# Optimization experiments

Hardware: AMD Instinct MI355X
Metric: run time of the kernel (lower is better)

## Reference

```python
import jax, jax.numpy as jnp
import numpy as np


def setup_inputs() -> dict:
    key = jax.random.key(0)
    k1, k2 = jax.random.split(key)
    B, N, D, O = 16, 2048, 512, 512
    x = jax.random.normal(k1, (B, N, D), dtype=jnp.float32)
    # original uses nn.init.uniform_ -> U[0,1)
    kernel = jax.random.uniform(k2, (3, D, O), dtype=jnp.float32)
    return {"x": x, "kernel": kernel}


def reference(x, kernel):
    # x: [B, N, D], kernel: [3, D, O]
    O = kernel.shape[-1]
    q = jnp.einsum("bnd,do->bno", x, kernel[0])
    k = jnp.einsum("bnd,do->bno", x, kernel[1])
    v = jnp.einsum("bnd,do->bno", x, kernel[2])
    scores = jnp.einsum("bqo,bko->bqk", q, k) / jnp.sqrt(jnp.float32(O))
    attn = jax.nn.softmax(scores, axis=-1)  # [B, N, N]
    return jnp.einsum("bqk,bko->bqo", attn, v)
```

## Files before the change

kernel.cpp:

```cpp
#include <hip/hip_runtime.h>
#include <hip/hip_bf16.h>

typedef __bf16 bf16_t;
typedef _Float16 f16_t;
typedef __bf16 bf16x8 __attribute__((ext_vector_type(8)));
typedef _Float16 f16x8 __attribute__((ext_vector_type(8)));
typedef float  f32x4  __attribute__((ext_vector_type(4)));

#define GAS __attribute__((address_space(1)))
#define LAS __attribute__((address_space(3)))

__device__ __forceinline__ void gload_lds16(const void* g, void* l) {
    __builtin_amdgcn_global_load_lds((const GAS void*)g, (LAS void*)l, 16, 0, 0);
}

#define QSCALE 0.044194173824159216f
#define L2E    1.4426950408889634f

__global__ __launch_bounds__(256) void k_split_x(const float* __restrict__ X,
                                                 bf16_t* __restrict__ H,
                                                 bf16_t* __restrict__ L, int n) {
    int i = (blockIdx.x * 256 + threadIdx.x) * 4;
    if (i >= n) return;
    float4 v = *(const float4*)(X + i);
    float vv[4] = {v.x, v.y, v.z, v.w};
    union { bf16_t b[4]; uint2 u; } hh, ll;
#pragma unroll
    for (int j = 0; j < 4; j++) {
        bf16_t h = (bf16_t)vv[j];
        hh.b[j] = h;
        ll.b[j] = (bf16_t)(vv[j] - (float)h);
    }
    *(uint2*)(H + i) = hh.u;
    *(uint2*)(L + i) = ll.u;
}

__global__ __launch_bounds__(256) void k_split_wt(const float* __restrict__ W,
                                                  bf16_t* __restrict__ H,
                                                  bf16_t* __restrict__ L) {
    int t = blockIdx.x * 256 + threadIdx.x;
    int base = t * 4;
    int m = base >> 18;
    int o = (base >> 9) & 511;
    int d = base & 511;
    union { bf16_t b[4]; uint2 u; } hh, ll;
#pragma unroll
    for (int j = 0; j < 4; j++) {
        float w = W[m * 262144 + (d + j) * 512 + o];
        bf16_t h = (bf16_t)w;
        hh.b[j] = h;
        ll.b[j] = (bf16_t)(w - (float)h);
    }
    *(uint2*)(H + base) = hh.u;
    *(uint2*)(L + base) = ll.u;
}

__global__ __launch_bounds__(256) void k_qkv(
    const bf16_t* __restrict__ Ah, const bf16_t* __restrict__ Al,
    const bf16_t* __restrict__ Bh, const bf16_t* __restrict__ Bl,
    f16_t* __restrict__ Qf,
    f16_t* __restrict__ Kh, f16_t* __restrict__ Kl,
    bf16_t* __restrict__ VT) {
    __shared__ bf16_t lds[16384];
    bf16_t* As_h = lds;
    bf16_t* Bs_h = lds + 4096;
    bf16_t* As_l = lds + 8192;
    bf16_t* Bs_l = lds + 12288;

    const int tid = threadIdx.x;
    const int lane = tid & 63;
    const int wid = tid >> 6;
    const int wr = wid >> 1, wc = wid & 1;
    const size_t i0 = (size_t)blockIdx.y * 128;
    const size_t j0 = (size_t)blockIdx.x * 128;

    const bf16_t* pAh = Ah + i0 * 512;
    const bf16_t* pBh = Bh + j0 * 512;
    const bf16_t* pAl = Al + i0 * 512;
    const bf16_t* pBl = Bl + j0 * 512;

    const int srow = tid >> 2;
    const int scoff = (tid & 3) * 8;

    f32x4 acc[4][4] = {};

    const int arow = wr * 64 + (lane & 15);
    const int brow = wc * 64 + (lane & 15);
    const int ko = (lane >> 4) * 8;

    for (int kt = 0; kt < 512; kt += 32) {
#pragma unroll
        for (int c = 0; c < 2; c++) {
            const size_t ra = (size_t)(c * 64 + srow) * 512 + kt + scoff;
            const int loff = c * 2048 + tid * 8;
            gload_lds16(pAh + ra, As_h + loff);
            gload_lds16(pBh + ra, Bs_h + loff);
            gload_lds16(pAl + ra, As_l + loff);
            gload_lds16(pBl + ra, Bs_l + loff);
        }
        __syncthreads();

        bf16x8 ah[4], bh[4], al[4], bl[4];
#pragma unroll
        for (int m = 0; m < 4; m++) ah[m] = *(const bf16x8*)&As_h[(arow + m * 16) * 32 + ko];
#pragma unroll
        for (int n = 0; n < 4; n++) bh[n] = *(const bf16x8*)&Bs_h[(brow + n * 16) * 32 + ko];
#pragma unroll
        for (int m = 0; m < 4; m++) al[m] = *(const bf16x8*)&As_l[(arow + m * 16) * 32 + ko];
#pragma unroll
        for (int n = 0; n < 4; n++) bl[n] = *(const bf16x8*)&Bs_l[(brow + n * 16) * 32 + ko];
        __builtin_amdgcn_s_setprio(1);
#pragma unroll
        for (int m = 0; m < 4; m++)
#pragma unroll
            for (int n = 0; n < 4; n++) {
                acc[m][n] = __builtin_amdgcn_mfma_f32_16x16x32_bf16(ah[m], bh[n], acc[m][n], 0, 0, 0);
                acc[m][n] = __builtin_amdgcn_mfma_f32_16x16x32_bf16(ah[m], bl[n], acc[m][n], 0, 0, 0);
                acc[m][n] = __builtin_amdgcn_mfma_f32_16x16x32_bf16(al[m], bh[n], acc[m][n], 0, 0, 0);
            }
        __builtin_amdgcn_s_setprio(0);
        __syncthreads();
    }

#pragma unroll
    for (int m = 0; m < 4; m++) {
#pragma unroll
        for (int n = 0; n < 4; n++) {
#pragma unroll
            for (int j = 0; j < 4; j++) {
                const size_t gr = i0 + wr * 64 + m * 16 + (lane >> 4) * 4 + j;
                const size_t gc = j0 + wc * 64 + n * 16 + (lane & 15);
                float v = acc[m][n][j];
                const int mat = (int)(gc >> 9);
                const size_t bloc = gr >> 11;
                const size_t nrow = gr & 2047;
                const size_t o = gc & 511;
                const size_t idx = bloc * 1048576 + nrow * 512 + o;
                if (mat == 0) {
                    Qf[idx] = (f16_t)(v * QSCALE);
                } else if (mat == 1) {
                    f16_t h = (f16_t)v;
                    Kh[idx] = h; Kl[idx] = (f16_t)(v - (float)h);
                } else {
                    VT[bloc * 1048576 + o * 2048 + nrow] = (bf16_t)v;
                }
            }
        }
    }
}

#define CH_SZ   24576
#define VT_OFF  49152
#define PT_OFF  114688
#define MP_OFF  122880
#define SP_OFF  123392
#define MR_OFF  123904

__global__ __launch_bounds__(512) void k_flash(
    const f16_t* __restrict__ Qf,
    const f16_t* __restrict__ Kh, const f16_t* __restrict__ Kl,
    const bf16_t* __restrict__ VT, float* __restrict__ Out) {
    __shared__ __align__(16) char smem[124416];

    const int tid = threadIdx.x;
    const int l = tid & 63, wid = tid >> 6;
    const int l15 = l & 15, l4 = l >> 4;
    const int rg4 = wid >> 1, kg = wid & 1;
    const int rg2 = wid >> 2, cg = wid & 3;

    const int total = gridDim.x * gridDim.y;
    const int f = blockIdx.x + gridDim.x * blockIdx.y;
    const int fp = (f & 7) * (total >> 3) + (f >> 3);
    const int b = fp >> 5;
    const int q0 = (fp & 31) * 64;
    const size_t NB = 1048576;

    const f16_t* qfb = Qf + (size_t)b * NB;
    const f16_t* khb = Kh + (size_t)b * NB;
    const f16_t* klb = Kl + (size_t)b * NB;
    const bf16_t* vtb = VT + (size_t)b * NB;

    float* MP = (float*)(smem + MP_OFF);
    float* SP = (float*)(smem + SP_OFF);
    float* MR = (float*)(smem + MR_OFF);

    if (tid < 128) MR[tid] = -3e38f;

    f32x4 O[2][8] = {};
    float mreg[2][4], lreg[2][4];
#pragma unroll
    for (int mf = 0; mf < 2; mf++)
#pragma unroll
        for (int j = 0; j < 4; j++) { mreg[mf][j] = -3e38f; lreg[mf][j] = 0.f; }

    const int srow = tid >> 3;
    const int sgl = (tid & 7) ^ (srow & 7);
    const int gsw = l15 & 7;

    auto stage_chunk = [&](int t, int kc, int b2) {
        const int co = kc * 64 + sgl * 8;
        f16_t* d = (f16_t*)(smem + b2 * CH_SZ) + tid * 8;
        gload_lds16(qfb + (size_t)(q0 + srow) * 512 + co, d);
        gload_lds16(khb + (size_t)(t * 64 + srow) * 512 + co, d + 4096);
        gload_lds16(klb + (size_t)(t * 64 + srow) * 512 + co, d + 8192);
    };
    auto stage_v = [&](int t, int j) {
        const int g = j * 512 + tid;
        const int orow = g >> 3;
        const int gl = (g & 7) ^ (orow & 7);
        gload_lds16(vtb + (size_t)orow * 2048 + t * 64 + gl * 8,
                    (bf16_t*)(smem + VT_OFF + g * 16));
    };

    stage_chunk(0, 0, 0);

#pragma unroll 1
    for (int t = 0; t < 32; t++) {
        f32x4 S[2] = {};
#pragma unroll
        for (int kc = 0; kc < 8; kc++) {
            if (kc == 0)      asm volatile("s_waitcnt vmcnt(0) lgkmcnt(0)" ::: "memory");
            else if (kc == 7) asm volatile("s_waitcnt vmcnt(2)" ::: "memory");
            else              asm volatile("s_waitcnt vmcnt(1)" ::: "memory");
            __builtin_amdgcn_s_barrier();
            if (kc < 7) {
                stage_chunk(t, kc + 1, (kc + 1) & 1);
                stage_v(t, kc);
                if (kc == 6) stage_v(t, 7);
            } else if (t < 31) {
                stage_chunk(t + 1, 0, 0);
            }
            const char* CB = smem + (kc & 1) * CH_SZ;
            const int arow = rg4 * 16 + l15;
#pragma unroll
            for (int ks = 0; ks < 2; ks++) {
                const int gph = ((ks * 4 + l4) ^ gsw) << 4;
                f16x8 qa = *(const f16x8*)(CB + arow * 128 + gph);
                __builtin_amdgcn_s_setprio(1);
#pragma unroll
                for (int nf = 0; nf < 2; nf++) {
                    const int brow = kg * 32 + nf * 16 + l15;
                    f16x8 bh = *(const f16x8*)(CB + 8192 + brow * 128 + gph);
                    f16x8 bl = *(const f16x8*)(CB + 16384 + brow * 128 + gph);
                    S[nf] = __builtin_amdgcn_mfma_f32_16x16x32_f16(qa, bh, S[nf], 0, 0, 0);
                    S[nf] = __builtin_amdgcn_mfma_f32_16x16x32_f16(qa, bl, S[nf], 0, 0, 0);
                }
                __builtin_amdgcn_s_setprio(0);
            }
        }

        const int rb4 = rg4 * 16 + l4 * 4;
        float pm[4];
#pragma unroll
        for (int j = 0; j < 4; j++) pm[j] = fmaxf(S[0][j], S[1][j]);
#pragma unroll
        for (int off = 1; off < 16; off <<= 1)
#pragma unroll
            for (int j = 0; j < 4; j++) pm[j] = fmaxf(pm[j], __shfl_xor(pm[j], off));
        if (l15 == 0) {
            f32x4 v; v[0] = pm[0]; v[1] = pm[1]; v[2] = pm[2]; v[3] = pm[3];
            *(f32x4*)(MP + kg * 64 + rb4) = v;
        }
        asm volatile("s_waitcnt lgkmcnt(0)" ::: "memory");
        __builtin_amdgcn_s_barrier();

        f32x4 mp0 = *(const f32x4*)(MP + rb4);
        f32x4 mp1 = *(const f32x4*)(MP + 64 + rb4);
        f32x4 mold = *(const f32x4*)(MR + (t & 1) * 64 + rb4);
        float mnew[4];
#pragma unroll
        for (int j = 0; j < 4; j++) mnew[j] = fmaxf(mold[j], fmaxf(mp0[j], mp1[j]));
        if (kg == 0 && l15 == 0) {
            f32x4 v; v[0] = mnew[0]; v[1] = mnew[1]; v[2] = mnew[2]; v[3] = mnew[3];
            *(f32x4*)(MR + ((t + 1) & 1) * 64 + rb4) = v;
        }
        float p[2][4], ps[4];
#pragma unroll
        for (int nf = 0; nf < 2; nf++)
#pragma unroll
            for (int j = 0; j < 4; j++) p[nf][j] = exp2f((S[nf][j] - mnew[j]) * L2E);
#pragma unroll
        for (int j = 0; j < 4; j++) ps[j] = p[0][j] + p[1][j];
#pragma unroll
        for (int off = 1; off < 16; off <<= 1)
#pragma unroll
            for (int j = 0; j < 4; j++) ps[j] += __shfl_xor(ps[j], off);
        if (l15 == 0) {
            f32x4 v; v[0] = ps[0]; v[1] = ps[1]; v[2] = ps[2]; v[3] = ps[3];
            *(f32x4*)(SP + kg * 64 + rb4) = v;
        }
#pragma unroll
        for (int nf = 0; nf < 2; nf++)
#pragma unroll
            for (int j = 0; j < 4; j++) {
                const int row = rb4 + j;
                const int phys = (kg * 4 + nf * 2 + (l15 >> 3)) ^ (row & 7);
                *(bf16_t*)(smem + PT_OFF + row * 128 + phys * 16 + (l15 & 7) * 2) =
                    (bf16_t)p[nf][j];
            }
        if (t < 31) asm volatile("s_waitcnt vmcnt(3) lgkmcnt(0)" ::: "memory");
        else        asm volatile("s_waitcnt vmcnt(0) lgkmcnt(0)" ::: "memory");
        __builtin_amdgcn_s_barrier();

#pragma unroll
        for (int mf = 0; mf < 2; mf++) {
            const int rb = rg2 * 32 + mf * 16 + l4 * 4;
            f32x4 mn = *(const f32x4*)(MR + ((t + 1) & 1) * 64 + rb);
            f32x4 sp0 = *(const f32x4*)(SP + rb);
            f32x4 sp1 = *(const f32x4*)(SP + 64 + rb);
            float fr[4];
#pragma unroll
            for (int j = 0; j < 4; j++) {
                fr[j] = exp2f((mreg[mf][j] - mn[j]) * L2E);
                lreg[mf][j] = lreg[mf][j] * fr[j] + sp0[j] + sp1[j];
                mreg[mf][j] = mn[j];
            }
#pragma unroll
            for (int nf = 0; nf < 8; nf++)
#pragma unroll
                for (int j = 0; j < 4; j++) O[mf][nf][j] *= fr[j];
        }
#pragma unroll
        for (int ks = 0; ks < 2; ks++) {
            const int gph = ((ks * 4 + l4) ^ gsw) << 4;
            bf16x8 pa[2];
#pragma unroll
            for (int mf = 0; mf < 2; mf++) {
                const int prow = rg2 * 32 + mf * 16 + l15;
                pa[mf] = *(const bf16x8*)(smem + PT_OFF + prow * 128 + gph);
            }
            __builtin_amdgcn_s_setprio(1);
#pragma unroll
            for (int nf = 0; nf < 8; nf++) {
                const int vrow = cg * 128 + nf * 16 + l15;
                bf16x8 vb = *(const bf16x8*)(smem + VT_OFF + vrow * 128 + gph);
#pragma unroll
                for (int mf = 0; mf < 2; mf++)
                    O[mf][nf] = __builtin_amdgcn_mfma_f32_16x16x32_bf16(pa[mf], vb, O[mf][nf], 0, 0, 0);
            }
            __builtin_amdgcn_s_setprio(0);
        }
    }

#pragma unroll
    for (int mf = 0; mf < 2; mf++) {
        float inv[4];
#pragma unroll
        for (int j = 0; j < 4; j++) inv[j] = 1.0f / lreg[mf][j];
#pragma unroll
        for (int nf = 0; nf < 8; nf++)
#pragma unroll
            for (int j = 0; j < 4; j++) {
                const size_t row = q0 + rg2 * 32 + mf * 16 + l4 * 4 + j;
                const size_t col = cg * 128 + nf * 16 + l15;
                Out[(size_t)b * NB + row * 512 + col] = O[mf][nf][j] * inv[j];
            }
    }
}

extern "C" void kernel_launch(void* const* d_in, const int* in_sizes, int n_in,
                              void* d_out, int out_size, void* d_ws, size_t ws_size,
                              hipStream_t stream) {
    const float* x = (const float*)d_in[0];
    const float* w = (const float*)d_in[1];
    float* out = (float*)d_out;

    const size_t NB = (size_t)2048 * 512;
    const size_t NW = (size_t)3 * 512 * 512;

    const size_t perG = 6 * NB * 2;
    size_t fixed = 2 * NW * 2 + 4096;
    int G = 1;
    if (ws_size > fixed + perG) {
        size_t g = (ws_size - fixed) / perG;
        G = (int)(g > 16 ? 16 : g);
    } else {
        return;
    }

    size_t off = 0;
    char* wsb = (char*)d_ws;
    auto take = [&](size_t bytes) -> char* {
        char* p = wsb + off;
        off = (off + bytes + 255) & ~(size_t)255;
        return p;
    };
    bf16_t* wth = (bf16_t*)take(NW * 2);
    bf16_t* wtl = (bf16_t*)take(NW * 2);
    bf16_t* xh = (bf16_t*)take(G * NB * 2);
    bf16_t* xl = (bf16_t*)take(G * NB * 2);
    f16_t*  qf = (f16_t*)take(G * NB * 2);
    f16_t*  kh = (f16_t*)take(G * NB * 2);
    f16_t*  kl = (f16_t*)take(G * NB * 2);
    bf16_t* vt = (bf16_t*)take(G * NB * 2);

    k_split_wt<<<dim3((unsigned)(NW / 4 / 256)), 256, 0, stream>>>(w, wth, wtl);

    for (int g0 = 0; g0 < 16; g0 += G) {
        const int Gc = (16 - g0 < G) ? (16 - g0) : G;
        const size_t base = (size_t)g0 * NB;
        k_split_x<<<dim3((unsigned)(Gc * NB / 4 / 256)), 256, 0, stream>>>(
            x + base, xh, xl, (int)(Gc * NB));
        k_qkv<<<dim3(12, 16 * Gc), 256, 0, stream>>>(
            xh, xl, wth, wtl, qf, kh, kl, vt);
        k_flash<<<dim3(32, Gc), 512, 0, stream>>>(
            qf, kh, kl, vt, out + base);
    }
}
```

Measured before the change: 651.1 us.

## Keep Q tile in registers and stage K in 128-wide double chunks

The Q tile is loaded once into registers (16 f16x8 fragments per lane) instead of being re-streamed from global into LDS for every key tile. K hi/lo staging now moves 128 columns per step, which halves the barrier and wait steps per key tile from 8 to 4, and the V staging and vmcnt counts are rescheduled to match. This cuts redundant Q global traffic and synchronisation, but adds register pressure at 512 threads and raises LDS use to about 140KB.

```diff
diff --git a/kernel.cpp b/kernel.cpp
--- a/kernel.cpp
+++ b/kernel.cpp
@@ -149,18 +149,18 @@
     }
 }
 
-#define CH_SZ   24576
-#define VT_OFF  49152
-#define PT_OFF  114688
-#define MP_OFF  122880
-#define SP_OFF  123392
-#define MR_OFF  123904
+#define KB_SZ   32768
+#define VT_OFF  65536
+#define PT_OFF  131072
+#define MP_OFF  139264
+#define SP_OFF  139776
+#define MR_OFF  140288
 
 __global__ __launch_bounds__(512) void k_flash(
     const f16_t* __restrict__ Qf,
     const f16_t* __restrict__ Kh, const f16_t* __restrict__ Kl,
     const bf16_t* __restrict__ VT, float* __restrict__ Out) {
-    __shared__ __align__(16) char smem[124416];
+    __shared__ __align__(16) char smem[140800];
 
     const int tid = threadIdx.x;
     const int l = tid & 63, wid = tid >> 6;
@@ -197,12 +197,14 @@
     const int sgl = (tid & 7) ^ (srow & 7);
     const int gsw = l15 & 7;
 
-    auto stage_chunk = [&](int t, int kc, int b2) {
-        const int co = kc * 64 + sgl * 8;
-        f16_t* d = (f16_t*)(smem + b2 * CH_SZ) + tid * 8;
-        gload_lds16(qfb + (size_t)(q0 + srow) * 512 + co, d);
-        gload_lds16(khb + (size_t)(t * 64 + srow) * 512 + co, d + 4096);
-        gload_lds16(klb + (size_t)(t * 64 + srow) * 512 + co, d + 8192);
+    auto stage_k = [&](int t, int kc2, int b2) {
+#pragma unroll
+        for (int sub = 0; sub < 2; sub++) {
+            const int co = kc2 * 128 + sub * 64 + sgl * 8;
+            f16_t* d = (f16_t*)(smem + b2 * KB_SZ + sub * 16384) + tid * 8;
+            gload_lds16(khb + (size_t)(t * 64 + srow) * 512 + co, d);
+            gload_lds16(klb + (size_t)(t * 64 + srow) * 512 + co, d + 4096);
+        }
     };
     auto stage_v = [&](int t, int j) {
         const int g = j * 512 + tid;
@@ -212,41 +214,63 @@
                     (bf16_t*)(smem + VT_OFF + g * 16));
     };
 
-    stage_chunk(0, 0, 0);
+#pragma unroll
+    for (int qc = 0; qc < 8; qc++) {
+        const int co = qc * 64 + sgl * 8;
+        gload_lds16(qfb + (size_t)(q0 + srow) * 512 + co,
+                    (f16_t*)(smem + VT_OFF + qc * 8192) + tid * 8);
+    }
+    stage_k(0, 0, 0);
+    asm volatile("s_waitcnt vmcnt(4)" ::: "memory");
+    __builtin_amdgcn_s_barrier();
+
+    f16x8 qreg[16];
+    const int arow = rg4 * 16 + l15;
+#pragma unroll
+    for (int qc = 0; qc < 8; qc++)
+#pragma unroll
+        for (int ks = 0; ks < 2; ks++) {
+            const int gph = ((ks * 4 + l4) ^ gsw) << 4;
+            qreg[qc * 2 + ks] = *(const f16x8*)(smem + VT_OFF + qc * 8192 + arow * 128 + gph);
+        }
+    asm volatile("s_waitcnt lgkmcnt(0)" ::: "memory");
+    __builtin_amdgcn_s_barrier();
 
 #pragma unroll 1
     for (int t = 0; t < 32; t++) {
         f32x4 S[2] = {};
 #pragma unroll
-        for (int kc = 0; kc < 8; kc++) {
-            if (kc == 0)      asm volatile("s_waitcnt vmcnt(0) lgkmcnt(0)" ::: "memory");
-            else if (kc == 7) asm volatile("s_waitcnt vmcnt(2)" ::: "memory");
-            else              asm volatile("s_waitcnt vmcnt(1)" ::: "memory");
+        for (int kc2 = 0; kc2 < 4; kc2++) {
+            if (kc2 == 0) asm volatile("s_waitcnt vmcnt(0)" ::: "memory");
+            else          asm volatile("s_waitcnt vmcnt(2)" ::: "memory");
             __builtin_amdgcn_s_barrier();
-            if (kc < 7) {
-                stage_chunk(t, kc + 1, (kc + 1) & 1);
-                stage_v(t, kc);
-                if (kc == 6) stage_v(t, 7);
-            } else if (t < 31) {
-                stage_chunk(t + 1, 0, 0);
-            }
-            const char* CB = smem + (kc & 1) * CH_SZ;
-            const int arow = rg4 * 16 + l15;
-#pragma unroll
-            for (int ks = 0; ks < 2; ks++) {
-                const int gph = ((ks * 4 + l4) ^ gsw) << 4;
-                f16x8 qa = *(const f16x8*)(CB + arow * 128 + gph);
-                __builtin_amdgcn_s_setprio(1);
-#pragma unroll
-                for (int nf = 0; nf < 2; nf++) {
-                    const int brow = kg * 32 + nf * 16 + l15;
-                    f16x8 bh = *(const f16x8*)(CB + 8192 + brow * 128 + gph);
-                    f16x8 bl = *(const f16x8*)(CB + 16384 + brow * 128 + gph);
-                    S[nf] = __builtin_amdgcn_mfma_f32_16x16x32_f16(qa, bh, S[nf], 0, 0, 0);
-                    S[nf] = __builtin_amdgcn_mfma_f32_16x16x32_f16(qa, bl, S[nf], 0, 0, 0);
+            if (kc2 < 3) {
+                stage_k(t, kc2 + 1, (kc2 + 1) & 1);
+                stage_v(t, kc2 * 2);
+                stage_v(t, kc2 * 2 + 1);
+            } else {
+                stage_v(t, 6);
+                stage_v(t, 7);
+                if (t < 31) stage_k(t + 1, 0, 0);
+            }
+            const char* CB = smem + (kc2 & 1) * KB_SZ;
+#pragma unroll
+            for (int sub = 0; sub < 2; sub++)
+#pragma unroll
+                for (int ks = 0; ks < 2; ks++) {
+                    const int gph = ((ks * 4 + l4) ^ gsw) << 4;
+                    f16x8 qa = qreg[kc2 * 4 + sub * 2 + ks];
+                    __builtin_amdgcn_s_setprio(1);
+#pragma unroll
+                    for (int nf = 0; nf < 2; nf++) {
+                        const int brow = kg * 32 + nf * 16 + l15;
+                        f16x8 bh = *(const f16x8*)(CB + sub * 16384 + brow * 128 + gph);
+                        f16x8 bl = *(const f16x8*)(CB + sub * 16384 + 8192 + brow * 128 + gph);
+                        S[nf] = __builtin_amdgcn_mfma_f32_16x16x32_f16(qa, bh, S[nf], 0, 0, 0);
+                        S[nf] = __builtin_amdgcn_mfma_f32_16x16x32_f16(qa, bl, S[nf], 0, 0, 0);
+                    }
+                    __builtin_amdgcn_s_setprio(0);
                 }
-                __builtin_amdgcn_s_setprio(0);
-            }
         }
 
         const int rb4 = rg4 * 16 + l4 * 4;
@@ -298,7 +322,7 @@
                 *(bf16_t*)(smem + PT_OFF + row * 128 + phys * 16 + (l15 & 7) * 2) =
                     (bf16_t)p[nf][j];
             }
-        if (t < 31) asm volatile("s_waitcnt vmcnt(3) lgkmcnt(0)" ::: "memory");
+        if (t < 31) asm volatile("s_waitcnt vmcnt(4) lgkmcnt(0)" ::: "memory");
         else        asm volatile("s_waitcnt vmcnt(0) lgkmcnt(0)" ::: "memory");
         __builtin_amdgcn_s_barrier();
 
```

New measurement: 568.1 us. 12.7% less time.
